# Performance work log

Measured on AMD Instinct MI355X. Metric: run time of the kernel, lower is better.

Reference implementation:

```python
import jax, jax.numpy as jnp
import numpy as np

TEMPERATURE = 8.0  # sqrt(d_k) with d_k = 64


def setup_inputs() -> dict:
    key = jax.random.key(0)
    ks = jax.random.split(key, 5)
    shape = (64, 1024, 64)  # [B*H, N, d_k]
    return {
        "q": jax.random.normal(ks[0], shape, dtype=jnp.float32),
        "k": jax.random.normal(ks[1], shape, dtype=jnp.float32),
        "v": jax.random.normal(ks[2], shape, dtype=jnp.float32),
        "q_sem": jax.random.normal(ks[3], shape, dtype=jnp.float32),
        "k_sem": jax.random.normal(ks[4], shape, dtype=jnp.float32),
    }


def reference(q, k, v, q_sem, k_sem):
    # Semantic fusion branch (q_sem is not None): scores are recomputed
    # with the fused queries/keys. (The original also computes an unused
    # softmax over the pre-fusion scores and an unused attn_sem bmm --
    # dead code with no effect on outputs, so omitted.)
    qf = q + q_sem
    kf = k + k_sem
    attn_score = jnp.einsum("bnd,bmd->bnm", qf, kf) / TEMPERATURE  # [BH, N, N]
    attn = jax.nn.softmax(attn_score, axis=2)
    # dropout in eval mode == identity
    output = jnp.einsum("bnm,bmd->bnd", attn, v)  # [BH, N, d_k]
    return (output, attn, attn_score)
```

## Files before the change

kernel.cpp:

```cpp
#include <hip/hip_runtime.h>
#include <math.h>


#define BH 64
#define N 1024
#define D 64
#define TM 64
#define TK 64
#define NC (N / TK)
#define KSTR 68
#define SSTR 68
#define LOG2E 1.44269504088896f
#define ESHIFT (-17.3123404907f)

typedef float    f32x4 __attribute__((ext_vector_type(4)));
typedef _Float16 half8 __attribute__((ext_vector_type(8)));
typedef _Float16 half4 __attribute__((ext_vector_type(4)));
typedef __fp16   fp16x2 __attribute__((ext_vector_type(2)));

__global__ __launch_bounds__(512, 4) void attn_fused_kernel(
    const float* __restrict__ q, const float* __restrict__ k,
    const float* __restrict__ v, const float* __restrict__ qsem,
    const float* __restrict__ ks, float* __restrict__ out_o,
    float* __restrict__ out_a, float* __restrict__ out_s)
{
    __shared__ __align__(16) _Float16 Kb[TK][KSTR];
    __shared__ __align__(16) _Float16 Vt[D][KSTR];
    __shared__ __align__(16) float    Sst[TM][SSTR];
    __shared__ float rsumf[TM];

    const int t  = threadIdx.x;
    const int w  = t >> 6;
    const int l  = t & 63;
    const int lr = l & 15;
    const int lg = l >> 4;
    const int qt = w >> 2;
    const int kt = w & 3;

    const int wg = blockIdx.x;
    const int b  = ((wg >> 7) << 3) | (wg & 7);
    const int q0 = ((wg >> 3) & 15) * TM;

    const size_t inb = (size_t)b * (N * D);
    const size_t sb  = (size_t)b * N * N + (size_t)q0 * N;

    half8 qa[2][2];
#pragma unroll
    for (int qs = 0; qs < 2; ++qs) {
        const float* qp  = q    + inb + (size_t)(q0 + (qt * 2 + qs) * 16 + lr) * D + lg * 8;
        const float* qsp = qsem + inb + (size_t)(q0 + (qt * 2 + qs) * 16 + lr) * D + lg * 8;
#pragma unroll
        for (int kst = 0; kst < 2; ++kst) {
            f32x4 a0 = *(const f32x4*)(qp + kst * 32);
            f32x4 a1 = *(const f32x4*)(qp + kst * 32 + 4);
            f32x4 c0 = *(const f32x4*)(qsp + kst * 32);
            f32x4 c1 = *(const f32x4*)(qsp + kst * 32 + 4);
            f32x4 s0 = a0 + c0, s1 = a1 + c1;
            union { half8 h8; fp16x2 h2[4]; } u;
            u.h2[0] = __builtin_amdgcn_cvt_pkrtz(s0[0], s0[1]);
            u.h2[1] = __builtin_amdgcn_cvt_pkrtz(s0[2], s0[3]);
            u.h2[2] = __builtin_amdgcn_cvt_pkrtz(s1[0], s1[1]);
            u.h2[3] = __builtin_amdgcn_cvt_pkrtz(s1[2], s1[3]);
            qa[qs][kst] = u.h8;
        }
    }

    const int  ts = t & 255;
    const bool kstager = (w < 4);

    auto STAGE = [&](int kc) {
        if (kstager) {
            const f32x4* kbp = (const f32x4*)(k  + inb + (size_t)kc * TK * D);
            const f32x4* sbp = (const f32x4*)(ks + inb + (size_t)kc * TK * D);
#pragma unroll
            for (int h = 0; h < 2; ++h) {
                f32x4 k0 = kbp[(2 * h)     * 256 + ts];
                f32x4 k1 = kbp[(2 * h + 1) * 256 + ts];
                f32x4 s0 = sbp[(2 * h)     * 256 + ts];
                f32x4 s1 = sbp[(2 * h + 1) * 256 + ts];
                f32x4 m0 = k0 + s0, m1 = k1 + s1;
                const int row0 = (2 * h) * 16 + (ts >> 4);
                const int col  = (ts & 15) * 4;
                union { half4 h4; fp16x2 h2[2]; } u0, u1;
                u0.h2[0] = __builtin_amdgcn_cvt_pkrtz(m0[0], m0[1]);
                u0.h2[1] = __builtin_amdgcn_cvt_pkrtz(m0[2], m0[3]);
                u1.h2[0] = __builtin_amdgcn_cvt_pkrtz(m1[0], m1[1]);
                u1.h2[1] = __builtin_amdgcn_cvt_pkrtz(m1[2], m1[3]);
                *(half4*)&Kb[row0][col]      = u0.h4;
                *(half4*)&Kb[row0 + 16][col] = u1.h4;
            }
        } else {
            const f32x4* vbp = (const f32x4*)(v + inb + (size_t)kc * TK * D);
            f32x4 vr0 = vbp[((ts >> 4) * 4 + 0) * 16 + (ts & 15)];
            f32x4 vr1 = vbp[((ts >> 4) * 4 + 1) * 16 + (ts & 15)];
            f32x4 vr2 = vbp[((ts >> 4) * 4 + 2) * 16 + (ts & 15)];
            f32x4 vr3 = vbp[((ts >> 4) * 4 + 3) * 16 + (ts & 15)];
            const int br4 = (ts >> 4) * 4, bc4 = (ts & 15) * 4;
#pragma unroll
            for (int c = 0; c < 4; ++c) {
                union { half4 h4; fp16x2 h2[2]; } u;
                u.h2[0] = __builtin_amdgcn_cvt_pkrtz(vr0[c], vr1[c]);
                u.h2[1] = __builtin_amdgcn_cvt_pkrtz(vr2[c], vr3[c]);
                *(half4*)&Vt[bc4 + c][br4] = u.h4;
            }
        }
    };

    f32x4 oacc[2];
    oacc[0] = (f32x4){0.f, 0.f, 0.f, 0.f};
    oacc[1] = (f32x4){0.f, 0.f, 0.f, 0.f};
    float rs[2] = {0.f, 0.f};

    for (int kc = 0; kc < NC; ++kc) {
        __syncthreads();
        STAGE(kc);
        __syncthreads();

        {
            half8 kb0 = *(const half8*)&Kb[kt * 16 + lr][lg * 8];
            half8 kb1 = *(const half8*)&Kb[kt * 16 + lr][32 + lg * 8];
#pragma unroll
            for (int qs = 0; qs < 2; ++qs) {
                f32x4 ac = {0.f, 0.f, 0.f, 0.f};
                ac = __builtin_amdgcn_mfma_f32_16x16x32_f16(qa[qs][0], kb0, ac, 0, 0, 0);
                ac = __builtin_amdgcn_mfma_f32_16x16x32_f16(qa[qs][1], kb1, ac, 0, 0, 0);
#pragma unroll
                for (int r = 0; r < 4; ++r)
                    Sst[(qt * 2 + qs) * 16 + lg * 4 + r][kt * 16 + lr] = ac[r] * 0.125f;
            }
        }
        __syncthreads();

#pragma unroll
        for (int h = 0; h < 2; ++h) {
            const int srow = h * 32 + (t >> 4);
            f32x4 sv = *(const f32x4*)&Sst[srow][(t & 15) * 4];
            *(f32x4*)(out_s + sb + (size_t)srow * N + kc * TK + (t & 15) * 4) = sv;
        }

#pragma unroll
        for (int kst = 0; kst < 2; ++kst) {
            half8 vb = *(const half8*)&Vt[kt * 16 + lr][kst * 32 + lg * 8];
#pragma unroll
            for (int qs = 0; qs < 2; ++qs) {
                const int prow = (qt * 2 + qs) * 16 + lr;
                f32x4 s0 = *(const f32x4*)&Sst[prow][kst * 32 + lg * 8];
                f32x4 s1 = *(const f32x4*)&Sst[prow][kst * 32 + lg * 8 + 4];
                float e0 = __builtin_amdgcn_exp2f(__builtin_fmaf(s0[0], LOG2E, ESHIFT));
                float e1 = __builtin_amdgcn_exp2f(__builtin_fmaf(s0[1], LOG2E, ESHIFT));
                float e2 = __builtin_amdgcn_exp2f(__builtin_fmaf(s0[2], LOG2E, ESHIFT));
                float e3 = __builtin_amdgcn_exp2f(__builtin_fmaf(s0[3], LOG2E, ESHIFT));
                float e4 = __builtin_amdgcn_exp2f(__builtin_fmaf(s1[0], LOG2E, ESHIFT));
                float e5 = __builtin_amdgcn_exp2f(__builtin_fmaf(s1[1], LOG2E, ESHIFT));
                float e6 = __builtin_amdgcn_exp2f(__builtin_fmaf(s1[2], LOG2E, ESHIFT));
                float e7 = __builtin_amdgcn_exp2f(__builtin_fmaf(s1[3], LOG2E, ESHIFT));
                if (kt == 0)
                    rs[qs] += ((e0 + e1) + (e2 + e3)) + ((e4 + e5) + (e6 + e7));
                union { half8 h8; fp16x2 h2[4]; } u;
                u.h2[0] = __builtin_amdgcn_cvt_pkrtz(e0, e1);
                u.h2[1] = __builtin_amdgcn_cvt_pkrtz(e2, e3);
                u.h2[2] = __builtin_amdgcn_cvt_pkrtz(e4, e5);
                u.h2[3] = __builtin_amdgcn_cvt_pkrtz(e6, e7);
                oacc[qs] = __builtin_amdgcn_mfma_f32_16x16x32_f16(u.h8, vb, oacc[qs], 0, 0, 0);
            }
        }
    }

    if (kt == 0) {
#pragma unroll
        for (int qs = 0; qs < 2; ++qs) {
            float x = rs[qs];
            x += __shfl_xor(x, 16);
            x += __shfl_xor(x, 32);
            if (l < 16) rsumf[(qt * 2 + qs) * 16 + l] = x;
        }
    }
    __syncthreads();
    if (t < TM) rsumf[t] = 1.0f / rsumf[t];
    __syncthreads();

#pragma unroll
    for (int qs = 0; qs < 2; ++qs)
#pragma unroll
    for (int r = 0; r < 4; ++r) {
        const int row = (qt * 2 + qs) * 16 + lg * 4 + r;
        Sst[row][kt * 16 + lr] = oacc[qs][r] * rsumf[row];
    }
    __syncthreads();
#pragma unroll
    for (int h = 0; h < 2; ++h) {
        const int srow = h * 32 + (t >> 4);
        f32x4 ov = *(const f32x4*)&Sst[srow][(t & 15) * 4];
        __builtin_nontemporal_store(ov,
            (f32x4*)(out_o + inb + (size_t)(q0 + srow) * D + (t & 15) * 4));
    }

#pragma unroll
    for (int h = 0; h < 2; ++h) {
        const int   arow = h * 32 + (t >> 4);
        const int   ac0  = (t & 15) * 4;
        const float iva  = rsumf[arow];
        const float* sp  = out_s + sb + (size_t)arow * N + ac0;
        float*       ap  = out_a + sb + (size_t)arow * N + ac0;
#pragma unroll 4
        for (int cb = 0; cb < NC; ++cb) {
            f32x4 sv = *(const f32x4*)(sp + cb * TK);
            f32x4 av;
#pragma unroll
            for (int i = 0; i < 4; ++i)
                av[i] = __builtin_amdgcn_exp2f(__builtin_fmaf(sv[i], LOG2E, ESHIFT)) * iva;
            __builtin_nontemporal_store(av, (f32x4*)(ap + cb * TK));
        }
    }
}

extern "C" void kernel_launch(void* const* d_in, const int* in_sizes, int n_in,
                              void* d_out, int out_size, void* d_ws, size_t ws_size,
                              hipStream_t stream) {
    const float* q  = (const float*)d_in[0];
    const float* k  = (const float*)d_in[1];
    const float* v  = (const float*)d_in[2];
    const float* qs = (const float*)d_in[3];
    const float* ks = (const float*)d_in[4];

    float* out_o = (float*)d_out;
    float* out_a = out_o + (size_t)BH * N * D;
    float* out_s = out_a + (size_t)BH * N * N;

    attn_fused_kernel<<<dim3(BH * (N / TM)), dim3(512), 0, stream>>>(
        q, k, v, qs, ks, out_o, out_a, out_s);
}
```

Before: 690.3 us.

## Double query tile per block to 128 rows with 1024-thread blocks

Each block now covers 128 query rows with 16 waves instead of 64 rows with 8 waves, so each staged K/V chunk is shared by twice as many query rows. The aim is to halve redundant global reads and fp16 conversion of K, K_sem and V across blocks. Staging is redistributed over 512 K-threads and 512 V-threads. The grid is half as large, and the larger blocks with a doubled score tile in shared memory may lower occupancy.

```diff
diff --git a/kernel.cpp b/kernel.cpp
--- a/kernel.cpp
+++ b/kernel.cpp
@@ -5,7 +5,7 @@
 #define BH 64
 #define N 1024
 #define D 64
-#define TM 64
+#define TM 128
 #define TK 64
 #define NC (N / TK)
 #define KSTR 68
@@ -18,7 +18,7 @@
 typedef _Float16 half4 __attribute__((ext_vector_type(4)));
 typedef __fp16   fp16x2 __attribute__((ext_vector_type(2)));
 
-__global__ __launch_bounds__(512, 4) void attn_fused_kernel(
+__global__ __launch_bounds__(1024, 4) void attn_fused_kernel(
     const float* __restrict__ q, const float* __restrict__ k,
     const float* __restrict__ v, const float* __restrict__ qsem,
     const float* __restrict__ ks, float* __restrict__ out_o,
@@ -34,12 +34,12 @@
     const int l  = t & 63;
     const int lr = l & 15;
     const int lg = l >> 4;
-    const int qt = w >> 2;
+    const int qp = w >> 2;
     const int kt = w & 3;
 
     const int wg = blockIdx.x;
-    const int b  = ((wg >> 7) << 3) | (wg & 7);
-    const int q0 = ((wg >> 3) & 15) * TM;
+    const int b  = ((wg >> 6) << 3) | (wg & 7);
+    const int q0 = ((wg >> 3) & 7) * TM;
 
     const size_t inb = (size_t)b * (N * D);
     const size_t sb  = (size_t)b * N * N + (size_t)q0 * N;
@@ -47,12 +47,12 @@
     half8 qa[2][2];
 #pragma unroll
     for (int qs = 0; qs < 2; ++qs) {
-        const float* qp  = q    + inb + (size_t)(q0 + (qt * 2 + qs) * 16 + lr) * D + lg * 8;
-        const float* qsp = qsem + inb + (size_t)(q0 + (qt * 2 + qs) * 16 + lr) * D + lg * 8;
+        const float* qp_  = q    + inb + (size_t)(q0 + (qp * 2 + qs) * 16 + lr) * D + lg * 8;
+        const float* qsp  = qsem + inb + (size_t)(q0 + (qp * 2 + qs) * 16 + lr) * D + lg * 8;
 #pragma unroll
         for (int kst = 0; kst < 2; ++kst) {
-            f32x4 a0 = *(const f32x4*)(qp + kst * 32);
-            f32x4 a1 = *(const f32x4*)(qp + kst * 32 + 4);
+            f32x4 a0 = *(const f32x4*)(qp_ + kst * 32);
+            f32x4 a1 = *(const f32x4*)(qp_ + kst * 32 + 4);
             f32x4 c0 = *(const f32x4*)(qsp + kst * 32);
             f32x4 c1 = *(const f32x4*)(qsp + kst * 32 + 4);
             f32x4 s0 = a0 + c0, s1 = a1 + c1;
@@ -65,44 +65,35 @@
         }
     }
 
-    const int  ts = t & 255;
-    const bool kstager = (w < 4);
+    const int  ts = t & 511;
+    const bool kstager = (w < 8);
 
     auto STAGE = [&](int kc) {
         if (kstager) {
             const f32x4* kbp = (const f32x4*)(k  + inb + (size_t)kc * TK * D);
             const f32x4* sbp = (const f32x4*)(ks + inb + (size_t)kc * TK * D);
 #pragma unroll
-            for (int h = 0; h < 2; ++h) {
-                f32x4 k0 = kbp[(2 * h)     * 256 + ts];
-                f32x4 k1 = kbp[(2 * h + 1) * 256 + ts];
-                f32x4 s0 = sbp[(2 * h)     * 256 + ts];
-                f32x4 s1 = sbp[(2 * h + 1) * 256 + ts];
-                f32x4 m0 = k0 + s0, m1 = k1 + s1;
-                const int row0 = (2 * h) * 16 + (ts >> 4);
-                const int col  = (ts & 15) * 4;
-                union { half4 h4; fp16x2 h2[2]; } u0, u1;
-                u0.h2[0] = __builtin_amdgcn_cvt_pkrtz(m0[0], m0[1]);
-                u0.h2[1] = __builtin_amdgcn_cvt_pkrtz(m0[2], m0[3]);
-                u1.h2[0] = __builtin_amdgcn_cvt_pkrtz(m1[0], m1[1]);
-                u1.h2[1] = __builtin_amdgcn_cvt_pkrtz(m1[2], m1[3]);
-                *(half4*)&Kb[row0][col]      = u0.h4;
-                *(half4*)&Kb[row0 + 16][col] = u1.h4;
+            for (int j = 0; j < 2; ++j) {
+                const int idx = j * 512 + ts;
+                f32x4 kk = kbp[idx];
+                f32x4 ss = sbp[idx];
+                f32x4 m  = kk + ss;
+                const int row = idx >> 4, col = (idx & 15) * 4;
+                union { half4 h4; fp16x2 h2[2]; } u;
+                u.h2[0] = __builtin_amdgcn_cvt_pkrtz(m[0], m[1]);
+                u.h2[1] = __builtin_amdgcn_cvt_pkrtz(m[2], m[3]);
+                *(half4*)&Kb[row][col] = u.h4;
             }
         } else {
             const f32x4* vbp = (const f32x4*)(v + inb + (size_t)kc * TK * D);
-            f32x4 vr0 = vbp[((ts >> 4) * 4 + 0) * 16 + (ts & 15)];
-            f32x4 vr1 = vbp[((ts >> 4) * 4 + 1) * 16 + (ts & 15)];
-            f32x4 vr2 = vbp[((ts >> 4) * 4 + 2) * 16 + (ts & 15)];
-            f32x4 vr3 = vbp[((ts >> 4) * 4 + 3) * 16 + (ts & 15)];
-            const int br4 = (ts >> 4) * 4, bc4 = (ts & 15) * 4;
-#pragma unroll
-            for (int c = 0; c < 4; ++c) {
-                union { half4 h4; fp16x2 h2[2]; } u;
-                u.h2[0] = __builtin_amdgcn_cvt_pkrtz(vr0[c], vr1[c]);
-                u.h2[1] = __builtin_amdgcn_cvt_pkrtz(vr2[c], vr3[c]);
-                *(half4*)&Vt[bc4 + c][br4] = u.h4;
-            }
+            const int br2 = (ts >> 4) * 2;
+            const int bc4 = (ts & 15) * 4;
+            f32x4 vr0 = vbp[(size_t)br2 * 16 + (ts & 15)];
+            f32x4 vr1 = vbp[(size_t)(br2 + 1) * 16 + (ts & 15)];
+#pragma unroll
+            for (int c = 0; c < 4; ++c)
+                *(fp16x2*)&Vt[bc4 + c][br2] =
+                    __builtin_amdgcn_cvt_pkrtz(vr0[c], vr1[c]);
         }
     };
 
@@ -126,14 +117,14 @@
                 ac = __builtin_amdgcn_mfma_f32_16x16x32_f16(qa[qs][1], kb1, ac, 0, 0, 0);
 #pragma unroll
                 for (int r = 0; r < 4; ++r)
-                    Sst[(qt * 2 + qs) * 16 + lg * 4 + r][kt * 16 + lr] = ac[r] * 0.125f;
+                    Sst[(qp * 2 + qs) * 16 + lg * 4 + r][kt * 16 + lr] = ac[r] * 0.125f;
             }
         }
         __syncthreads();
 
 #pragma unroll
         for (int h = 0; h < 2; ++h) {
-            const int srow = h * 32 + (t >> 4);
+            const int srow = h * 64 + (t >> 4);
             f32x4 sv = *(const f32x4*)&Sst[srow][(t & 15) * 4];
             *(f32x4*)(out_s + sb + (size_t)srow * N + kc * TK + (t & 15) * 4) = sv;
         }
@@ -143,7 +134,7 @@
             half8 vb = *(const half8*)&Vt[kt * 16 + lr][kst * 32 + lg * 8];
 #pragma unroll
             for (int qs = 0; qs < 2; ++qs) {
-                const int prow = (qt * 2 + qs) * 16 + lr;
+                const int prow = (qp * 2 + qs) * 16 + lr;
                 f32x4 s0 = *(const f32x4*)&Sst[prow][kst * 32 + lg * 8];
                 f32x4 s1 = *(const f32x4*)&Sst[prow][kst * 32 + lg * 8 + 4];
                 float e0 = __builtin_amdgcn_exp2f(__builtin_fmaf(s0[0], LOG2E, ESHIFT));
@@ -172,7 +163,7 @@
             float x = rs[qs];
             x += __shfl_xor(x, 16);
             x += __shfl_xor(x, 32);
-            if (l < 16) rsumf[(qt * 2 + qs) * 16 + l] = x;
+            if (l < 16) rsumf[(qp * 2 + qs) * 16 + l] = x;
         }
     }
     __syncthreads();
@@ -183,13 +174,13 @@
     for (int qs = 0; qs < 2; ++qs)
 #pragma unroll
     for (int r = 0; r < 4; ++r) {
-        const int row = (qt * 2 + qs) * 16 + lg * 4 + r;
+        const int row = (qp * 2 + qs) * 16 + lg * 4 + r;
         Sst[row][kt * 16 + lr] = oacc[qs][r] * rsumf[row];
     }
     __syncthreads();
 #pragma unroll
     for (int h = 0; h < 2; ++h) {
-        const int srow = h * 32 + (t >> 4);
+        const int srow = h * 64 + (t >> 4);
         f32x4 ov = *(const f32x4*)&Sst[srow][(t & 15) * 4];
         __builtin_nontemporal_store(ov,
             (f32x4*)(out_o + inb + (size_t)(q0 + srow) * D + (t & 15) * 4));
@@ -197,7 +188,7 @@
 
 #pragma unroll
     for (int h = 0; h < 2; ++h) {
-        const int   arow = h * 32 + (t >> 4);
+        const int   arow = h * 64 + (t >> 4);
         const int   ac0  = (t & 15) * 4;
         const float iva  = rsumf[arow];
         const float* sp  = out_s + sb + (size_t)arow * N + ac0;
@@ -227,6 +218,6 @@
     float* out_a = out_o + (size_t)BH * N * D;
     float* out_s = out_a + (size_t)BH * N * N;
 
-    attn_fused_kernel<<<dim3(BH * (N / TM)), dim3(512), 0, stream>>>(
+    attn_fused_kernel<<<dim3(BH * (N / TM)), dim3(1024), 0, stream>>>(
         q, k, v, qs, ks, out_o, out_a, out_s);
 }
```

Result: no change. 677.4 us (-1.9%).
